# Performance work log

Measured on AMD Instinct MI355X. Metric: run time of the kernel, lower is better.

Reference implementation:

```python
import jax, jax.numpy as jnp
import numpy as np

NUM_ITERATIONS = 3


def squash(s, axis):
    # s: capsule vectors; squash along `axis` (capsule dim)
    mag_sq = jnp.sum(s * s, axis=axis, keepdims=True)
    mag = jnp.sqrt(mag_sq)
    return mag_sq / (1.0 + mag_sq) * (s / mag)


def setup_inputs() -> dict:
    key = jax.random.key(0)
    k1, k2 = jax.random.split(key)
    B, IN_SIZE, I = 256, 8, 1152   # batch, in_size, in_node_num
    N, O = 10, 16                  # num_node, node_size
    x = jax.random.normal(k1, (B, IN_SIZE, I), dtype=jnp.float32)
    W = jax.random.normal(k2, (1, I, N, O, IN_SIZE), dtype=jnp.float32)
    return {"x": x, "W": W}


def reference(x, W):
    # x: (B, in_size, I); W: (1, I, N, O, in_size)
    B = x.shape[0]
    I, N = W.shape[1], W.shape[2]
    xt = jnp.swapaxes(x, 1, 2)  # (B, I, in_size)
    # u_hat[b,i,n,o] = sum_k (0.03*W[0,i,n,o,k]) * x[b,i,k]
    u_hat = jnp.einsum('inok,bik->bino', W[0] * 0.03, xt)  # (B, I, N, O)
    b_ij = jnp.zeros((I, N), dtype=x.dtype)
    v_j = None
    for _ in range(NUM_ITERATIONS):
        c_ij = jax.nn.softmax(b_ij, axis=1)              # softmax over num_node
        s_j = jnp.einsum('in,bino->bno', c_ij, u_hat)    # (B, N, O)
        v_j = squash(s_j, axis=-1)                       # squash over node_size
        # agreement: u_hat . v_j, averaged over batch
        u_vj = jnp.einsum('bino,bno->bin', u_hat, v_j).mean(axis=0)  # (I, N)
        b_ij = b_ij + u_vj
    return v_j[:, :, :, None]  # (B, N, O, 1) == v_j.squeeze(1) in torch
```

## Files before the change

### kernel.cpp

```cpp
#include <hip/hip_runtime.h>

#define B_   256
#define I_   1152
#define N_   10
#define P_   9216
#define NO_  160

typedef unsigned short u16;
typedef short s8v __attribute__((ext_vector_type(8)));
typedef float f4v __attribute__((ext_vector_type(4)));

__device__ inline float bf2f(u16 u){
  unsigned v = ((unsigned)u) << 16; float f; __builtin_memcpy(&f, &v, 4); return f;
}
__device__ inline u16 f2bf(float f){
  unsigned b; __builtin_memcpy(&b, &f, 4);
  b += 0x7fffu + ((b >> 16) & 1u);
  return (u16)(b >> 16);
}

__global__ void k_prep(const float* __restrict__ x, const float* __restrict__ W,
                       u16* __restrict__ xbp, u16* __restrict__ xpb,
                       u16* __restrict__ Wt, float* __restrict__ bij,
                       float* __restrict__ sA){
  __shared__ float tile[32][36];
  int t = threadIdx.x, u = blockIdx.x;
  if (u < 800){
    if (u < 45) bij[u*256 + t] = 0.f;
    else if (u < 205) sA[(u - 45)*256 + t] = 0.f;
    int q = u / 5, ic = u - (u/5)*5;
    int n = q >> 4, o = q & 15;
    int i = ic*256 + t;
    if (i < I_){
      const float* src = W + (size_t)i*1280 + n*128 + o*8;
      float4 a = *reinterpret_cast<const float4*>(src);
      float4 b = *reinterpret_cast<const float4*>(src + 4);
      float vv[8] = {a.x,a.y,a.z,a.w,b.x,b.y,b.z,b.w};
      #pragma unroll
      for (int k = 0; k < 8; ++k)
        Wt[(size_t)q*P_ + (size_t)k*I_ + i] = f2bf(vv[k] * 0.03f);
    }
  } else {
    int b2 = u - 800;
    int tb = b2 & 7, tp = b2 >> 3;
    int b0 = tb << 5, p0 = tp << 5;
    int r = t >> 3, c4 = (t & 7) << 2;
    float4 v = *reinterpret_cast<const float4*>(x + (size_t)(b0 + r)*P_ + p0 + c4);
    *reinterpret_cast<float4*>(&tile[r][c4]) = v;
    uint2 pk;
    pk.x = (unsigned)f2bf(v.x) | ((unsigned)f2bf(v.y) << 16);
    pk.y = (unsigned)f2bf(v.z) | ((unsigned)f2bf(v.w) << 16);
    *reinterpret_cast<uint2*>(xbp + (size_t)(b0 + r)*P_ + p0 + c4) = pk;
    __syncthreads();
    float f0 = tile[c4+0][r], f1 = tile[c4+1][r], f2 = tile[c4+2][r], f3 = tile[c4+3][r];
    uint2 pk2;
    pk2.x = (unsigned)f2bf(f0) | ((unsigned)f2bf(f1) << 16);
    pk2.y = (unsigned)f2bf(f2) | ((unsigned)f2bf(f3) << 16);
    *reinterpret_cast<uint2*>(xpb + (size_t)(p0 + r)*B_ + b0 + c4) = pk2;
  }
}

__global__ __launch_bounds__(128) void k_s2a(
    const u16* __restrict__ xbp, const u16* __restrict__ Wt,
    const float* __restrict__ bij, float* __restrict__ s_cur,
    float* __restrict__ s_next){
  __shared__ u16  Bt[16][592];
  __shared__ float c_lds[576];
  int t = threadIdx.x;
  int bx2 = blockIdx.x, n = blockIdx.y, kc = blockIdx.z;
  int lin = bx2 + 8*n + 80*kc;
  if (t < 32) s_next[lin*32 + t] = 0.f;
  int i0 = (kc & 1) * 576;

  for (int j = t; j < 576; j += 128){
    const float* br = bij + (size_t)(i0 + j)*N_;
    float l0 = br[0], l1 = br[1], l2 = br[2], l3 = br[3], l4 = br[4];
    float l5 = br[5], l6 = br[6], l7 = br[7], l8 = br[8], l9 = br[9];
    float mx = fmaxf(fmaxf(fmaxf(fmaxf(l0,l1),fmaxf(l2,l3)),
                           fmaxf(fmaxf(l4,l5),fmaxf(l6,l7))), fmaxf(l8,l9));
    float e0=__expf(l0-mx), e1=__expf(l1-mx), e2=__expf(l2-mx), e3=__expf(l3-mx), e4=__expf(l4-mx);
    float e5=__expf(l5-mx), e6=__expf(l6-mx), e7=__expf(l7-mx), e8=__expf(l8-mx), e9=__expf(l9-mx);
    float se = e0+e1+e2+e3+e4+e5+e6+e7+e8+e9;
    float ev[10] = {e0,e1,e2,e3,e4,e5,e6,e7,e8,e9};
    c_lds[j] = ev[n] / se;
  }
  __syncthreads();

  for (int u = t; u < 1152; u += 128){
    int r = u / 72, cb = (u - r*72) * 8;
    uint4 w = *reinterpret_cast<const uint4*>(Wt + (size_t)(n*16 + r)*P_ + kc*576 + cb);
    float4 c0 = *reinterpret_cast<const float4*>(&c_lds[cb]);
    float4 c1 = *reinterpret_cast<const float4*>(&c_lds[cb + 4]);
    uint4 rr;
    rr.x = (unsigned)f2bf(bf2f(w.x & 0xffff)*c0.x) | ((unsigned)f2bf(bf2f(w.x >> 16)*c0.y) << 16);
    rr.y = (unsigned)f2bf(bf2f(w.y & 0xffff)*c0.z) | ((unsigned)f2bf(bf2f(w.y >> 16)*c0.w) << 16);
    rr.z = (unsigned)f2bf(bf2f(w.z & 0xffff)*c1.x) | ((unsigned)f2bf(bf2f(w.z >> 16)*c1.y) << 16);
    rr.w = (unsigned)f2bf(bf2f(w.w & 0xffff)*c1.z) | ((unsigned)f2bf(bf2f(w.w >> 16)*c1.w) << 16);
    *reinterpret_cast<uint4*>(&Bt[r][cb]) = rr;
  }
  __syncthreads();

  int w = t >> 6, l = t & 63;
  int lo = l & 15, quad = l >> 4;
  int b0 = bx2*32 + w*16;
  const s8v* ap = reinterpret_cast<const s8v*>(xbp + (size_t)(b0 + lo)*P_ + kc*576 + quad*8);
  f4v acc0 = {0.f,0.f,0.f,0.f}, acc1 = {0.f,0.f,0.f,0.f};
  #pragma unroll
  for (int s = 0; s < 9; ++s){
    s8v a0 = ap[8*s];
    s8v b0v = *reinterpret_cast<const s8v*>(&Bt[lo][quad*8 + 64*s]);
    s8v a1 = ap[8*s + 4];
    s8v b1v = *reinterpret_cast<const s8v*>(&Bt[lo][quad*8 + 64*s + 32]);
    acc0 = __builtin_amdgcn_mfma_f32_16x16x32_bf16(a0, b0v, acc0, 0, 0, 0);
    acc1 = __builtin_amdgcn_mfma_f32_16x16x32_bf16(a1, b1v, acc1, 0, 0, 0);
  }
  f4v acc = acc0 + acc1;
  int r0 = quad << 2;
  #pragma unroll
  for (int r = 0; r < 4; ++r)
    atomicAdd(&s_cur[(size_t)(b0 + r0 + r)*NO_ + n*16 + lo], acc[r]);
}

__global__ __launch_bounds__(256, 4) void k_g2(
    const u16* __restrict__ xpb, const float* __restrict__ s,
    const u16* __restrict__ Wt, float* __restrict__ bij){
  __shared__ u16 vl[32][264];
  int t = threadIdx.x;
  int qp = blockIdx.x / 144;
  int b = t;
  #pragma unroll
  for (int nn = 0; nn < 2; ++nn){
    const float* sr = s + (size_t)b*NO_ + (qp*2 + nn)*16;
    float4 s0 = *reinterpret_cast<const float4*>(sr);
    float4 s1 = *reinterpret_cast<const float4*>(sr + 4);
    float4 s2 = *reinterpret_cast<const float4*>(sr + 8);
    float4 s3 = *reinterpret_cast<const float4*>(sr + 12);
    float sq = s0.x*s0.x+s0.y*s0.y+s0.z*s0.z+s0.w*s0.w
             + s1.x*s1.x+s1.y*s1.y+s1.z*s1.z+s1.w*s1.w
             + s2.x*s2.x+s2.y*s2.y+s2.z*s2.z+s2.w*s2.w
             + s3.x*s3.x+s3.y*s3.y+s3.z*s3.z+s3.w*s3.w;
    float scale = sqrtf(sq) / (1.0f + sq);
    float sv[16] = {s0.x,s0.y,s0.z,s0.w,s1.x,s1.y,s1.z,s1.w,
                    s2.x,s2.y,s2.z,s2.w,s3.x,s3.y,s3.z,s3.w};
    #pragma unroll
    for (int o = 0; o < 16; ++o)
      vl[nn*16 + o][b] = f2bf(sv[o] * scale);
  }
  __syncthreads();

  int wv = t >> 6, l = t & 63;
  int pt = (blockIdx.x % 144)*4 + wv;
  int p0 = pt << 4;
  int lo = l & 15, quad = l >> 4;
  const s8v* ap = reinterpret_cast<const s8v*>(xpb + (size_t)(p0 + lo)*B_ + quad*8);
  f4v acc0 = {0.f,0.f,0.f,0.f}, acc1 = {0.f,0.f,0.f,0.f};
  #pragma unroll
  for (int st = 0; st < 8; ++st){
    s8v a  = ap[4*st];
    s8v b0 = *reinterpret_cast<const s8v*>(&vl[lo]     [st*32 + quad*8]);
    s8v b1 = *reinterpret_cast<const s8v*>(&vl[16 + lo][st*32 + quad*8]);
    acc0 = __builtin_amdgcn_mfma_f32_16x16x32_bf16(a, b0, acc0, 0, 0, 0);
    acc1 = __builtin_amdgcn_mfma_f32_16x16x32_bf16(a, b1, acc1, 0, 0, 0);
  }
  int ib = p0 % 1152;
  #pragma unroll
  for (int sb = 0; sb < 2; ++sb){
    f4v acc = sb ? acc1 : acc0;
    int n = qp*2 + sb;
    const u16* wp = Wt + (size_t)(n*16 + lo)*P_ + p0 + (quad << 2);
    ushort4 w4 = *reinterpret_cast<const ushort4*>(wp);
    float v0 = acc[0]*bf2f(w4.x), v1 = acc[1]*bf2f(w4.y);
    float v2 = acc[2]*bf2f(w4.z), v3 = acc[3]*bf2f(w4.w);
    #pragma unroll
    for (int m = 8; m >= 1; m >>= 1){
      v0 += __shfl_xor(v0, m, 16);
      v1 += __shfl_xor(v1, m, 16);
      v2 += __shfl_xor(v2, m, 16);
      v3 += __shfl_xor(v3, m, 16);
    }
    if (lo == 0){
      int i = ib + (quad << 2);
      atomicAdd(&bij[(i+0)*N_ + n], v0 * (1.f/256.f));
      atomicAdd(&bij[(i+1)*N_ + n], v1 * (1.f/256.f));
      atomicAdd(&bij[(i+2)*N_ + n], v2 * (1.f/256.f));
      atomicAdd(&bij[(i+3)*N_ + n], v3 * (1.f/256.f));
    }
  }
}

__global__ void k_sqout(const float* __restrict__ s, float* __restrict__ out){
  int t = threadIdx.x;
  int o = t & 15, rl = t >> 4;
  int rowid = blockIdx.x*16 + rl;
  int b = rowid / 10, n = rowid - b*10;
  size_t idx = (size_t)b*NO_ + n*16 + o;
  float sv = s[idx];
  float sq = sv * sv;
  #pragma unroll
  for (int m = 8; m >= 1; m >>= 1) sq += __shfl_xor(sq, m, 16);
  out[idx] = sv * sqrtf(sq) / (1.0f + sq);
}

extern "C" void kernel_launch(void* const* d_in, const int* in_sizes, int n_in,
                              void* d_out, int out_size, void* d_ws, size_t ws_size,
                              hipStream_t stream){
  (void)in_sizes; (void)n_in; (void)out_size; (void)ws_size;
  const float* x = (const float*)d_in[0];
  const float* W = (const float*)d_in[1];
  float* out = (float*)d_out;

  float* sA  = (float*)d_ws;
  float* sB  = sA + 40960;
  float* bij = sB + 40960;
  u16* xbp = (u16*)(bij + 11520);
  u16* xpb = xbp + 2359296;
  u16* Wt  = xpb + 2359296;

  k_prep<<<3104, 256, 0, stream>>>(x, W, xbp, xpb, Wt, bij, sA);
  k_s2a<<<dim3(8, 10, 16), 128, 0, stream>>>(xbp, Wt, bij, sA, sB);
  k_g2 <<<720, 256, 0, stream>>>(xpb, sA, Wt, bij);
  k_s2a<<<dim3(8, 10, 16), 128, 0, stream>>>(xbp, Wt, bij, sB, sA);
  k_g2 <<<720, 256, 0, stream>>>(xpb, sB, Wt, bij);
  k_s2a<<<dim3(8, 10, 16), 128, 0, stream>>>(xbp, Wt, bij, sA, sB);
  k_sqout<<<160, 256, 0, stream>>>(sA, out);
}
```

Measured before the change: 132.2 us.

## Fuse routing iterations into one persistent kernel with hierarchical grid barrier

Replaces the five routing kernel launches and the final squash launch with one persistent kernel of 1280 blocks. Phases are separated by a two-level atomic grid barrier. The first iteration uses the uniform softmax constant 0.1 directly and skips the coefficient-scaling LDS staging. The G phase is restructured so each block handles work via a strided loop. This removes launch gaps and tail effects, but the barrier adds spin-wait cost and relies on all 1280 blocks being co-resident, which risks deadlock if occupancy is insufficient.

```diff
diff --git a/kernel.cpp b/kernel.cpp
--- a/kernel.cpp
+++ b/kernel.cpp
@@ -5,6 +5,7 @@
 #define N_   10
 #define P_   9216
 #define NO_  160
+#define NBLK 1280
 
 typedef unsigned short u16;
 typedef short s8v __attribute__((ext_vector_type(8)));
@@ -22,10 +23,13 @@
 __global__ void k_prep(const float* __restrict__ x, const float* __restrict__ W,
                        u16* __restrict__ xbp, u16* __restrict__ xpb,
                        u16* __restrict__ Wt, float* __restrict__ bij,
-                       float* __restrict__ sA){
+                       float* __restrict__ sA, int* __restrict__ bar){
   __shared__ float tile[32][36];
   int t = threadIdx.x, u = blockIdx.x;
   if (u < 800){
+    if (u == 0){
+      for (int z = t; z < 576; z += 256) bar[z] = 0;
+    }
     if (u < 45) bij[u*256 + t] = 0.f;
     else if (u < 205) sA[(u - 45)*256 + t] = 0.f;
     int q = u / 5, ic = u - (u/5)*5;
@@ -60,16 +64,38 @@
   }
 }
 
-__global__ __launch_bounds__(128) void k_s2a(
+__device__ inline void gbar(int* bar, int bid){
+  __syncthreads();
+  if (threadIdx.x == 0){
+    int* gen = bar + 544;
+    int g = __hip_atomic_load(gen, __ATOMIC_SEQ_CST, __HIP_MEMORY_SCOPE_AGENT);
+    int* leaf = bar + ((bid & 15) << 5);
+    if (__hip_atomic_fetch_add(leaf, 1, __ATOMIC_SEQ_CST, __HIP_MEMORY_SCOPE_AGENT) == 79){
+      __hip_atomic_store(leaf, 0, __ATOMIC_SEQ_CST, __HIP_MEMORY_SCOPE_AGENT);
+      if (__hip_atomic_fetch_add(bar + 512, 1, __ATOMIC_SEQ_CST, __HIP_MEMORY_SCOPE_AGENT) == 15){
+        __hip_atomic_store(bar + 512, 0, __ATOMIC_SEQ_CST, __HIP_MEMORY_SCOPE_AGENT);
+        __hip_atomic_fetch_add(gen, 1, __ATOMIC_SEQ_CST, __HIP_MEMORY_SCOPE_AGENT);
+      }
+    }
+    while (__hip_atomic_load(gen, __ATOMIC_RELAXED, __HIP_MEMORY_SCOPE_AGENT) == g)
+      __builtin_amdgcn_s_sleep(2);
+    __builtin_amdgcn_fence(__ATOMIC_ACQUIRE, "agent");
+  }
+  __syncthreads();
+}
+
+union LdsU {
+  struct { u16 Bt[16][592]; float c[576]; } S;
+  u16 vl[32][264];
+};
+
+__device__ inline void phase_S(int t, int bid,
     const u16* __restrict__ xbp, const u16* __restrict__ Wt,
     const float* __restrict__ bij, float* __restrict__ s_cur,
-    float* __restrict__ s_next){
-  __shared__ u16  Bt[16][592];
-  __shared__ float c_lds[576];
-  int t = threadIdx.x;
-  int bx2 = blockIdx.x, n = blockIdx.y, kc = blockIdx.z;
-  int lin = bx2 + 8*n + 80*kc;
-  if (t < 32) s_next[lin*32 + t] = 0.f;
+    float* __restrict__ s_zero, LdsU* lds)
+{
+  int bx2 = bid & 7, n = (bid >> 3) % 10, kc = bid / 80;
+  if (s_zero && t < 32) s_zero[bid*32 + t] = 0.f;
   int i0 = (kc & 1) * 576;
 
   for (int j = t; j < 576; j += 128){
@@ -82,35 +108,34 @@
     float e5=__expf(l5-mx), e6=__expf(l6-mx), e7=__expf(l7-mx), e8=__expf(l8-mx), e9=__expf(l9-mx);
     float se = e0+e1+e2+e3+e4+e5+e6+e7+e8+e9;
     float ev[10] = {e0,e1,e2,e3,e4,e5,e6,e7,e8,e9};
-    c_lds[j] = ev[n] / se;
+    lds->S.c[j] = ev[n] / se;
   }
   __syncthreads();
 
   for (int u = t; u < 1152; u += 128){
     int r = u / 72, cb = (u - r*72) * 8;
     uint4 w = *reinterpret_cast<const uint4*>(Wt + (size_t)(n*16 + r)*P_ + kc*576 + cb);
-    float4 c0 = *reinterpret_cast<const float4*>(&c_lds[cb]);
-    float4 c1 = *reinterpret_cast<const float4*>(&c_lds[cb + 4]);
+    float4 c0 = *reinterpret_cast<const float4*>(&lds->S.c[cb]);
+    float4 c1 = *reinterpret_cast<const float4*>(&lds->S.c[cb + 4]);
     uint4 rr;
     rr.x = (unsigned)f2bf(bf2f(w.x & 0xffff)*c0.x) | ((unsigned)f2bf(bf2f(w.x >> 16)*c0.y) << 16);
     rr.y = (unsigned)f2bf(bf2f(w.y & 0xffff)*c0.z) | ((unsigned)f2bf(bf2f(w.y >> 16)*c0.w) << 16);
     rr.z = (unsigned)f2bf(bf2f(w.z & 0xffff)*c1.x) | ((unsigned)f2bf(bf2f(w.z >> 16)*c1.y) << 16);
     rr.w = (unsigned)f2bf(bf2f(w.w & 0xffff)*c1.z) | ((unsigned)f2bf(bf2f(w.w >> 16)*c1.w) << 16);
-    *reinterpret_cast<uint4*>(&Bt[r][cb]) = rr;
-  }
-  __syncthreads();
-
-  int w = t >> 6, l = t & 63;
-  int lo = l & 15, quad = l >> 4;
-  int b0 = bx2*32 + w*16;
+    *reinterpret_cast<uint4*>(&lds->S.Bt[r][cb]) = rr;
+  }
+  __syncthreads();
+
+  int wid = t >> 6, l = t & 63, lo = l & 15, quad = l >> 4;
+  int b0 = bx2*32 + wid*16;
   const s8v* ap = reinterpret_cast<const s8v*>(xbp + (size_t)(b0 + lo)*P_ + kc*576 + quad*8);
   f4v acc0 = {0.f,0.f,0.f,0.f}, acc1 = {0.f,0.f,0.f,0.f};
   #pragma unroll
   for (int s = 0; s < 9; ++s){
     s8v a0 = ap[8*s];
-    s8v b0v = *reinterpret_cast<const s8v*>(&Bt[lo][quad*8 + 64*s]);
+    s8v b0v = *reinterpret_cast<const s8v*>(&lds->S.Bt[lo][quad*8 + 64*s]);
     s8v a1 = ap[8*s + 4];
-    s8v b1v = *reinterpret_cast<const s8v*>(&Bt[lo][quad*8 + 64*s + 32]);
+    s8v b1v = *reinterpret_cast<const s8v*>(&lds->S.Bt[lo][quad*8 + 64*s + 32]);
     acc0 = __builtin_amdgcn_mfma_f32_16x16x32_bf16(a0, b0v, acc0, 0, 0, 0);
     acc1 = __builtin_amdgcn_mfma_f32_16x16x32_bf16(a1, b1v, acc1, 0, 0, 0);
   }
@@ -121,84 +146,128 @@
     atomicAdd(&s_cur[(size_t)(b0 + r0 + r)*NO_ + n*16 + lo], acc[r]);
 }
 
-__global__ __launch_bounds__(256, 4) void k_g2(
+__device__ inline void phase_G(int t, int bid,
     const u16* __restrict__ xpb, const float* __restrict__ s,
-    const u16* __restrict__ Wt, float* __restrict__ bij){
-  __shared__ u16 vl[32][264];
-  int t = threadIdx.x;
-  int qp = blockIdx.x / 144;
-  int b = t;
+    const u16* __restrict__ Wt, float* __restrict__ bij, LdsU* lds)
+{
+  int qp = bid >> 8;
   #pragma unroll
-  for (int nn = 0; nn < 2; ++nn){
-    const float* sr = s + (size_t)b*NO_ + (qp*2 + nn)*16;
-    float4 s0 = *reinterpret_cast<const float4*>(sr);
-    float4 s1 = *reinterpret_cast<const float4*>(sr + 4);
-    float4 s2 = *reinterpret_cast<const float4*>(sr + 8);
-    float4 s3 = *reinterpret_cast<const float4*>(sr + 12);
-    float sq = s0.x*s0.x+s0.y*s0.y+s0.z*s0.z+s0.w*s0.w
-             + s1.x*s1.x+s1.y*s1.y+s1.z*s1.z+s1.w*s1.w
-             + s2.x*s2.x+s2.y*s2.y+s2.z*s2.z+s2.w*s2.w
-             + s3.x*s3.x+s3.y*s3.y+s3.z*s3.z+s3.w*s3.w;
-    float scale = sqrtf(sq) / (1.0f + sq);
-    float sv[16] = {s0.x,s0.y,s0.z,s0.w,s1.x,s1.y,s1.z,s1.w,
-                    s2.x,s2.y,s2.z,s2.w,s3.x,s3.y,s3.z,s3.w};
-    #pragma unroll
-    for (int o = 0; o < 16; ++o)
-      vl[nn*16 + o][b] = f2bf(sv[o] * scale);
-  }
-  __syncthreads();
-
-  int wv = t >> 6, l = t & 63;
-  int pt = (blockIdx.x % 144)*4 + wv;
-  int p0 = pt << 4;
-  int lo = l & 15, quad = l >> 4;
-  const s8v* ap = reinterpret_cast<const s8v*>(xpb + (size_t)(p0 + lo)*B_ + quad*8);
-  f4v acc0 = {0.f,0.f,0.f,0.f}, acc1 = {0.f,0.f,0.f,0.f};
-  #pragma unroll
-  for (int st = 0; st < 8; ++st){
-    s8v a  = ap[4*st];
-    s8v b0 = *reinterpret_cast<const s8v*>(&vl[lo]     [st*32 + quad*8]);
-    s8v b1 = *reinterpret_cast<const s8v*>(&vl[16 + lo][st*32 + quad*8]);
-    acc0 = __builtin_amdgcn_mfma_f32_16x16x32_bf16(a, b0, acc0, 0, 0, 0);
-    acc1 = __builtin_amdgcn_mfma_f32_16x16x32_bf16(a, b1, acc1, 0, 0, 0);
-  }
-  int ib = p0 % 1152;
-  #pragma unroll
-  for (int sb = 0; sb < 2; ++sb){
-    f4v acc = sb ? acc1 : acc0;
-    int n = qp*2 + sb;
-    const u16* wp = Wt + (size_t)(n*16 + lo)*P_ + p0 + (quad << 2);
-    ushort4 w4 = *reinterpret_cast<const ushort4*>(wp);
-    float v0 = acc[0]*bf2f(w4.x), v1 = acc[1]*bf2f(w4.y);
-    float v2 = acc[2]*bf2f(w4.z), v3 = acc[3]*bf2f(w4.w);
-    #pragma unroll
-    for (int m = 8; m >= 1; m >>= 1){
-      v0 += __shfl_xor(v0, m, 16);
-      v1 += __shfl_xor(v1, m, 16);
-      v2 += __shfl_xor(v2, m, 16);
-      v3 += __shfl_xor(v3, m, 16);
-    }
-    if (lo == 0){
-      int i = ib + (quad << 2);
-      atomicAdd(&bij[(i+0)*N_ + n], v0 * (1.f/256.f));
-      atomicAdd(&bij[(i+1)*N_ + n], v1 * (1.f/256.f));
-      atomicAdd(&bij[(i+2)*N_ + n], v2 * (1.f/256.f));
-      atomicAdd(&bij[(i+3)*N_ + n], v3 * (1.f/256.f));
-    }
-  }
-}
-
-__global__ void k_sqout(const float* __restrict__ s, float* __restrict__ out){
-  int t = threadIdx.x;
-  int o = t & 15, rl = t >> 4;
-  int rowid = blockIdx.x*16 + rl;
-  int b = rowid / 10, n = rowid - b*10;
-  size_t idx = (size_t)b*NO_ + n*16 + o;
-  float sv = s[idx];
-  float sq = sv * sv;
-  #pragma unroll
-  for (int m = 8; m >= 1; m >>= 1) sq += __shfl_xor(sq, m, 16);
-  out[idx] = sv * sqrtf(sq) / (1.0f + sq);
+  for (int h = 0; h < 2; ++h){
+    int b = t + h*128;
+    #pragma unroll
+    for (int nn = 0; nn < 2; ++nn){
+      const float* sr = s + (size_t)b*NO_ + (qp*2 + nn)*16;
+      float4 s0 = *reinterpret_cast<const float4*>(sr);
+      float4 s1 = *reinterpret_cast<const float4*>(sr + 4);
+      float4 s2 = *reinterpret_cast<const float4*>(sr + 8);
+      float4 s3 = *reinterpret_cast<const float4*>(sr + 12);
+      float sq = s0.x*s0.x+s0.y*s0.y+s0.z*s0.z+s0.w*s0.w
+               + s1.x*s1.x+s1.y*s1.y+s1.z*s1.z+s1.w*s1.w
+               + s2.x*s2.x+s2.y*s2.y+s2.z*s2.z+s2.w*s2.w
+               + s3.x*s3.x+s3.y*s3.y+s3.z*s3.z+s3.w*s3.w;
+      float scale = sqrtf(sq) / (1.0f + sq);
+      float sv[16] = {s0.x,s0.y,s0.z,s0.w,s1.x,s1.y,s1.z,s1.w,
+                      s2.x,s2.y,s2.z,s2.w,s3.x,s3.y,s3.z,s3.w};
+      #pragma unroll
+      for (int o = 0; o < 16; ++o)
+        lds->vl[nn*16 + o][b] = f2bf(sv[o] * scale);
+    }
+  }
+  __syncthreads();
+
+  int wv = t >> 6, l = t & 63, lo = l & 15, quad = l >> 4;
+  for (int u = (bid & 255)*2 + wv; u < 576; u += 512){
+    int p0 = u << 4;
+    const s8v* ap = reinterpret_cast<const s8v*>(xpb + (size_t)(p0 + lo)*B_ + quad*8);
+    f4v acc0 = {0.f,0.f,0.f,0.f}, acc1 = {0.f,0.f,0.f,0.f};
+    #pragma unroll
+    for (int st = 0; st < 8; ++st){
+      s8v a  = ap[4*st];
+      s8v b0 = *reinterpret_cast<const s8v*>(&lds->vl[lo]     [st*32 + quad*8]);
+      s8v b1 = *reinterpret_cast<const s8v*>(&lds->vl[16 + lo][st*32 + quad*8]);
+      acc0 = __builtin_amdgcn_mfma_f32_16x16x32_bf16(a, b0, acc0, 0, 0, 0);
+      acc1 = __builtin_amdgcn_mfma_f32_16x16x32_bf16(a, b1, acc1, 0, 0, 0);
+    }
+    int ib = p0 % 1152;
+    #pragma unroll
+    for (int sb = 0; sb < 2; ++sb){
+      f4v acc = sb ? acc1 : acc0;
+      int n = qp*2 + sb;
+      const u16* wp = Wt + (size_t)(n*16 + lo)*P_ + p0 + (quad << 2);
+      ushort4 w4 = *reinterpret_cast<const ushort4*>(wp);
+      float v0 = acc[0]*bf2f(w4.x), v1 = acc[1]*bf2f(w4.y);
+      float v2 = acc[2]*bf2f(w4.z), v3 = acc[3]*bf2f(w4.w);
+      #pragma unroll
+      for (int m = 8; m >= 1; m >>= 1){
+        v0 += __shfl_xor(v0, m, 16);
+        v1 += __shfl_xor(v1, m, 16);
+        v2 += __shfl_xor(v2, m, 16);
+        v3 += __shfl_xor(v3, m, 16);
+      }
+      if (lo == 0){
+        int i = ib + (quad << 2);
+        atomicAdd(&bij[(i+0)*N_ + n], v0 * (1.f/256.f));
+        atomicAdd(&bij[(i+1)*N_ + n], v1 * (1.f/256.f));
+        atomicAdd(&bij[(i+2)*N_ + n], v2 * (1.f/256.f));
+        atomicAdd(&bij[(i+3)*N_ + n], v3 * (1.f/256.f));
+      }
+    }
+  }
+}
+
+__global__ __launch_bounds__(128, 4) void k_route(
+    const u16* __restrict__ xbp, const u16* __restrict__ xpb,
+    const u16* __restrict__ Wt, float* __restrict__ bij,
+    float* __restrict__ sA, float* __restrict__ sB,
+    float* __restrict__ out, int* __restrict__ bar)
+{
+  __shared__ LdsU lds;
+  int t = threadIdx.x, bid = blockIdx.x;
+
+  {
+    int bx2 = bid & 7, n = (bid >> 3) % 10, kc = bid / 80;
+    if (t < 32) sB[bid*32 + t] = 0.f;
+    int wid = t >> 6, l = t & 63, lo = l & 15, quad = l >> 4;
+    int b0 = bx2*32 + wid*16;
+    const s8v* ap = reinterpret_cast<const s8v*>(xbp + (size_t)(b0 + lo)*P_ + kc*576 + quad*8);
+    const s8v* bp = reinterpret_cast<const s8v*>(Wt  + (size_t)(n*16 + lo)*P_ + kc*576 + quad*8);
+    f4v acc0 = {0.f,0.f,0.f,0.f}, acc1 = {0.f,0.f,0.f,0.f};
+    #pragma unroll
+    for (int s = 0; s < 9; ++s){
+      acc0 = __builtin_amdgcn_mfma_f32_16x16x32_bf16(ap[8*s],     bp[8*s],     acc0, 0, 0, 0);
+      acc1 = __builtin_amdgcn_mfma_f32_16x16x32_bf16(ap[8*s + 4], bp[8*s + 4], acc1, 0, 0, 0);
+    }
+    f4v acc = acc0 + acc1;
+    int r0 = quad << 2;
+    #pragma unroll
+    for (int r = 0; r < 4; ++r)
+      atomicAdd(&sA[(size_t)(b0 + r0 + r)*NO_ + n*16 + lo], acc[r] * 0.1f);
+  }
+  gbar(bar, bid);
+
+  phase_G(t, bid, xpb, sA, Wt, bij, &lds);
+  gbar(bar, bid);
+
+  phase_S(t, bid, xbp, Wt, bij, sB, sA, &lds);
+  gbar(bar, bid);
+
+  phase_G(t, bid, xpb, sB, Wt, bij, &lds);
+  gbar(bar, bid);
+
+  phase_S(t, bid, xbp, Wt, bij, sA, nullptr, &lds);
+  gbar(bar, bid);
+
+  if (bid < 320){
+    int o = t & 15, rl = t >> 4;
+    int rowid = bid*8 + rl;
+    int b = rowid / 10, n = rowid - b*10;
+    size_t idx = (size_t)b*NO_ + n*16 + o;
+    float sv = sA[idx];
+    float sq = sv * sv;
+    #pragma unroll
+    for (int m = 8; m >= 1; m >>= 1) sq += __shfl_xor(sq, m, 16);
+    out[idx] = sv * sqrtf(sq) / (1.0f + sq);
+  }
 }
 
 extern "C" void kernel_launch(void* const* d_in, const int* in_sizes, int n_in,
@@ -215,12 +284,8 @@
   u16* xbp = (u16*)(bij + 11520);
   u16* xpb = xbp + 2359296;
   u16* Wt  = xpb + 2359296;
-
-  k_prep<<<3104, 256, 0, stream>>>(x, W, xbp, xpb, Wt, bij, sA);
-  k_s2a<<<dim3(8, 10, 16), 128, 0, stream>>>(xbp, Wt, bij, sA, sB);
-  k_g2 <<<720, 256, 0, stream>>>(xpb, sA, Wt, bij);
-  k_s2a<<<dim3(8, 10, 16), 128, 0, stream>>>(xbp, Wt, bij, sB, sA);
-  k_g2 <<<720, 256, 0, stream>>>(xpb, sB, Wt, bij);
-  k_s2a<<<dim3(8, 10, 16), 128, 0, stream>>>(xbp, Wt, bij, sA, sB);
-  k_sqout<<<160, 256, 0, stream>>>(sA, out);
-}
+  int* bar = (int*)(Wt + 1474560);
+
+  k_prep<<<3104, 256, 0, stream>>>(x, W, xbp, xpb, Wt, bij, sA, bar);
+  k_route<<<NBLK, 128, 0, stream>>>(xbp, xpb, Wt, bij, sA, sB, out, bar);
+}
```

Measured after the change: 366.9 us. 2.78x slower.
